# Kernel tuning notes

Hardware: AMD Instinct MI355X
Metric: run time of the kernel (lower is better)

The kernel has to match this reference:

```python
import jax, jax.numpy as jnp
import numpy as np

B, L, D, H = 4, 2048, 1024, 16
DK = D // H


def setup_inputs() -> dict:
    key = jax.random.key(0)
    ks = jax.random.split(key, 8)
    def n(k, shape, s=1.0):
        return jax.random.normal(k, shape, dtype=jnp.float32) * s
    return {
        "q": n(ks[0], (B, L, D)),
        "k": n(ks[1], (B, L, D)),
        "v": n(ks[2], (B, L, D)),
        "Wq": n(ks[3], (D, D), 0.02), "bq": jnp.zeros((D,), jnp.float32),
        "Wk": n(ks[4], (D, D), 0.02), "bk": jnp.zeros((D,), jnp.float32),
        "Wv": n(ks[5], (D, D), 0.02), "bv": jnp.zeros((D,), jnp.float32),
        "Wo": n(ks[6], (D, D), 0.02), "bo": jnp.zeros((D,), jnp.float32),
        # relative-position table, torch: nn.Parameter(zeros(2L-1, d_k)); random here
        "w_rel": n(ks[7], (2 * L - 1, DK), 0.02),
    }


def reference(q, k, v, Wq, bq, Wk, bk, Wv, bv, Wo, bo, w_rel):
    # Dropout is identity in eval mode (reference baseline).
    bs, Lq, _ = q.shape
    qh = (q @ Wq.T + bq).reshape(bs, Lq, H, DK).transpose(0, 2, 1, 3)  # (B,H,L,dk)
    kh = (k @ Wk.T + bk).reshape(bs, -1, H, DK).transpose(0, 2, 1, 3)
    vh = (v @ Wv.T + bv).reshape(bs, -1, H, DK).transpose(0, 2, 1, 3)

    # content-content scores
    scores = jnp.einsum('bhid,bhjd->bhij', qh, kh)  # (B,H,L,L)

    # relative bias. torch unfold: rel_pos[i, d, j] = w_rel[i + j, d]
    # bias[b,h,i,j] = sum_d qh[b,h,i,d] * w_rel[i+j, d]
    # Compute t = q . w_rel over the 2L-1 axis, then skew-gather (avoids LxLxdk tensor).
    t = jnp.einsum('bhid,rd->bhir', qh, w_rel)  # (B,H,L,2L-1)
    idx = jnp.arange(Lq)[:, None] + jnp.arange(Lq)[None, :]  # (L,L) values i+j
    bias = jnp.take_along_axis(t, idx[None, None], axis=-1)  # (B,H,L,L)

    attn = jax.nn.softmax((scores + bias) / jnp.sqrt(jnp.float32(DK)), axis=-1)
    out = jnp.einsum('bhij,bhjd->bhid', attn, vh)  # (B,H,L,dk)
    concat = out.transpose(0, 2, 1, 3).reshape(bs, Lq, D)
    return concat @ Wo.T + bo
```

## Files before the change

### kernel.cpp

```cpp
#include <hip/hip_runtime.h>

typedef __attribute__((ext_vector_type(8))) short bf16x8;
typedef __attribute__((ext_vector_type(4))) float f32x4;
typedef unsigned short u16;
typedef unsigned int u32;

constexpr int kB = 4, kL = 2048, kD = 1024, kH = 16, kDK = 64;
constexpr int kR = kB * kL;
constexpr long kWrelMax = 2 * kL - 2;
constexpr float kQScale = 0.125f * 1.44269504088896f;
constexpr float kM = 12.0f;

__device__ inline float fexp2(float x) { return __builtin_amdgcn_exp2f(x); }

__device__ inline u16 f2bf(float x) {
    union { float f; u32 u; } v; v.f = x;
    u32 r = v.u + 0x7FFFu + ((v.u >> 16) & 1u);
    return (u16)(r >> 16);
}
__device__ inline float bf2f(u16 h) {
    union { u32 u; float f; } v; v.u = ((u32)h) << 16;
    return v.f;
}
__device__ inline void splitf(float x, u16& hi, u16& lo) {
    hi = f2bf(x);
    lo = f2bf(x - bf2f(hi));
}
__device__ inline f32x4 MFMA(bf16x8 a, bf16x8 b, f32x4 c) {
    return __builtin_amdgcn_mfma_f32_16x16x32_bf16(a, b, c, 0, 0, 0);
}
__device__ __forceinline__ void gll16(const u16* g, u16* l) {
    __builtin_amdgcn_global_load_lds(
        (const __attribute__((address_space(1))) u32*)g,
        (__attribute__((address_space(3))) u32*)l, 16, 0, 0);
}

__global__ void split4_kernel(const float* __restrict__ in,
                              u16* __restrict__ hi, u16* __restrict__ lo, int n4) {
    int idx = blockIdx.x * blockDim.x + threadIdx.x;
    if (idx >= n4) return;
    float4 x = reinterpret_cast<const float4*>(in)[idx];
    ushort4 h, l;
    splitf(x.x, h.x, l.x); splitf(x.y, h.y, l.y);
    splitf(x.z, h.z, l.z); splitf(x.w, h.w, l.w);
    reinterpret_cast<ushort4*>(hi)[idx] = h;
    reinterpret_cast<ushort4*>(lo)[idx] = l;
}

template<int AMODE, int OMODE, int TERMS>
__global__ __launch_bounds__(256) void mfma_gemm(
    const float* __restrict__ Af32,
    const u16* __restrict__ Agh, const u16* __restrict__ Agl,
    const u16* __restrict__ Bgh, const u16* __restrict__ Bgl,
    const float* __restrict__ bias, float scale,
    float* __restrict__ Yf, u16* __restrict__ Yh, u16* __restrict__ Yl)
{
    __shared__ __align__(16) u16 Ash[128 * 32], Asl[128 * 32];
    __shared__ __align__(16) u16 Bsh[128 * 32];
    __shared__ __align__(16) u16 Bsl[TERMS == 3 ? 128 * 32 : 8];

    const int tid = threadIdx.x;
    const int row0 = blockIdx.x * 128, col0 = blockIdx.y * 128;
    const int w = tid >> 6, lane = tid & 63;
    const int s = lane & 15, g = lane >> 4;
    const int wrow = w >> 1, wcol = w & 1;
    const int srow = tid >> 1;
    const int skq  = (tid & 1) * 16;

    const f32x4 fz = {0.f, 0.f, 0.f, 0.f};
    f32x4 acc[4][4];
    #pragma unroll
    for (int m = 0; m < 4; ++m)
        #pragma unroll
        for (int n = 0; n < 4; ++n) acc[m][n] = fz;

    float4 aR[4];
    bf16x8 aRh[2], aRl[2], bRh[2], bRl[2];

    auto loadA = [&](int k0) {
        if (AMODE == 0) {
            const float* p = &Af32[(size_t)(row0 + srow) * kD + k0 + skq];
            aR[0] = *(const float4*)(p);
            aR[1] = *(const float4*)(p + 4);
            aR[2] = *(const float4*)(p + 8);
            aR[3] = *(const float4*)(p + 12);
        } else {
            const u16* ph = &Agh[(size_t)(row0 + srow) * kD + k0 + skq];
            const u16* pl = &Agl[(size_t)(row0 + srow) * kD + k0 + skq];
            aRh[0] = *(const bf16x8*)ph; aRh[1] = *(const bf16x8*)(ph + 8);
            aRl[0] = *(const bf16x8*)pl; aRl[1] = *(const bf16x8*)(pl + 8);
        }
    };
    auto loadB = [&](int k0) {
        const u16* ph = &Bgh[(size_t)(col0 + srow) * kD + k0 + skq];
        bRh[0] = *(const bf16x8*)ph; bRh[1] = *(const bf16x8*)(ph + 8);
        if (TERMS == 3) {
            const u16* pl = &Bgl[(size_t)(col0 + srow) * kD + k0 + skq];
            bRl[0] = *(const bf16x8*)pl; bRl[1] = *(const bf16x8*)(pl + 8);
        }
    };
    auto writeAB = [&]() {
        const int c0 = skq >> 3, sw = srow & 3;
        bf16x8 h0, h1, l0, l1;
        if (AMODE == 0) {
            const float* af = (const float*)aR;
            #pragma unroll
            for (int q = 0; q < 8; ++q) {
                u16 hh, ll;
                splitf(af[q], hh, ll);     h0[q] = (short)hh; l0[q] = (short)ll;
                splitf(af[8 + q], hh, ll); h1[q] = (short)hh; l1[q] = (short)ll;
            }
        } else { h0 = aRh[0]; h1 = aRh[1]; l0 = aRl[0]; l1 = aRl[1]; }
        *(bf16x8*)&Ash[srow * 32 + (((c0    ) ^ sw) << 3)] = h0;
        *(bf16x8*)&Ash[srow * 32 + (((c0 + 1) ^ sw) << 3)] = h1;
        *(bf16x8*)&Asl[srow * 32 + (((c0    ) ^ sw) << 3)] = l0;
        *(bf16x8*)&Asl[srow * 32 + (((c0 + 1) ^ sw) << 3)] = l1;
        *(bf16x8*)&Bsh[srow * 32 + (((c0    ) ^ sw) << 3)] = bRh[0];
        *(bf16x8*)&Bsh[srow * 32 + (((c0 + 1) ^ sw) << 3)] = bRh[1];
        if (TERMS == 3) {
            *(bf16x8*)&Bsl[srow * 32 + (((c0    ) ^ sw) << 3)] = bRl[0];
            *(bf16x8*)&Bsl[srow * 32 + (((c0 + 1) ^ sw) << 3)] = bRl[1];
        }
    };

    loadA(0); loadB(0);
    for (int k0 = 0; k0 < kD; k0 += 32) {
        __syncthreads();
        writeAB();
        __syncthreads();
        if (k0 + 32 < kD) { loadA(k0 + 32); loadB(k0 + 32); }

        bf16x8 fAh[4], fAl[4], fBh[4], fBl[4];
        #pragma unroll
        for (int m = 0; m < 4; ++m) {
            int ar = wrow * 64 + m * 16 + s;
            int off = ar * 32 + ((g ^ (ar & 3)) << 3);
            fAh[m] = *(const bf16x8*)&Ash[off];
            fAl[m] = *(const bf16x8*)&Asl[off];
        }
        #pragma unroll
        for (int n = 0; n < 4; ++n) {
            int bc = wcol * 64 + n * 16 + s;
            int off = bc * 32 + ((g ^ (bc & 3)) << 3);
            fBh[n] = *(const bf16x8*)&Bsh[off];
            if (TERMS == 3) fBl[n] = *(const bf16x8*)&Bsl[off];
        }
        #pragma unroll
        for (int m = 0; m < 4; ++m)
            #pragma unroll
            for (int n = 0; n < 4; ++n) {
                acc[m][n] = MFMA(fAh[m], fBh[n], acc[m][n]);
                acc[m][n] = MFMA(fAl[m], fBh[n], acc[m][n]);
                if (TERMS == 3) acc[m][n] = MFMA(fAh[m], fBl[n], acc[m][n]);
            }
    }

    #pragma unroll
    for (int n = 0; n < 4; ++n) {
        const int colg = col0 + wcol * 64 + n * 16 + s;
        const float bv = bias[colg];
        #pragma unroll
        for (int m = 0; m < 4; ++m) {
            const int rowg = row0 + wrow * 64 + m * 16 + (g << 2);
            #pragma unroll
            for (int r = 0; r < 4; ++r) {
                float val = (acc[m][n][r] + bv) * scale;
                if (OMODE == 1) {
                    Yf[(size_t)(rowg + r) * kD + colg] = val;
                } else {
                    const int rg = rowg + r;
                    const int b = rg >> 11, i = rg & (kL - 1);
                    const int h = colg >> 6, d = colg & 63;
                    size_t o = (((size_t)b * kH + h) * kL + i) * kDK + d;
                    if (OMODE == 0) { u16 hh, ll; splitf(val, hh, ll); Yh[o] = hh; Yl[o] = ll; }
                    else             { Yh[o] = f2bf(val); }
                }
            }
        }
    }
}

__global__ __launch_bounds__(256) void transpose64(const u16* __restrict__ src,
                                                   u16* __restrict__ dst) {
    __shared__ u16 tls[64][72];
    const int tid = threadIdx.x;
    const int bh = blockIdx.y, j0 = blockIdx.x * 64;
    const int jr = tid >> 2, d0 = (tid & 3) * 16;
    const u16* p = src + ((size_t)bh * kL + j0 + jr) * kDK + d0;
    *(bf16x8*)&tls[jr][d0]     = *(const bf16x8*)p;
    *(bf16x8*)&tls[jr][d0 + 8] = *(const bf16x8*)(p + 8);
    __syncthreads();
    const int dr = tid >> 2, jc = (tid & 3) * 16;
    __align__(16) u16 tmp[16];
    #pragma unroll
    for (int q = 0; q < 16; ++q) tmp[q] = tls[jc + q][dr];
    u16* pd = dst + ((size_t)bh * kDK + dr) * kL + j0 + jc;
    *(bf16x8*)pd       = *(const bf16x8*)&tmp[0];
    *(bf16x8*)(pd + 8) = *(const bf16x8*)&tmp[8];
}

__global__ __launch_bounds__(256, 2) void attn3(
    const u16* __restrict__ Qh,
    const u16* __restrict__ Kg, const u16* __restrict__ VT,
    const u16* __restrict__ Wr,
    u16* __restrict__ Ch, u16* __restrict__ Cl)
{
    __shared__ __align__(16) u16 Ksh[2][64 * 64];
    __shared__ __align__(16) u16 Vsh[2][64 * 64];
    __shared__ __align__(16) u16 Wsh[2][64 * 64];
    __shared__ __align__(16) u16 Ps[4][16 * 64];
    __shared__ __align__(16) u16 Tb[4][128 * 20];

    const int tid = threadIdx.x;
    const int w = tid >> 6, lane = tid & 63;
    const int s = lane & 15, g = lane >> 4;
    const int bh = blockIdx.y, i0 = blockIdx.x * 64;
    const int b = bh >> 4, h = bh & 15;

    const int srow = tid >> 3;
    const int sc = tid & 7;

    auto stageK = [&](int buf, int t) {
        const u16* base = Kg + ((size_t)bh * kL + (size_t)t * 64) * kDK;
        #pragma unroll
        for (int it = 0; it < 2; ++it) {
            int r = srow + it * 32;
            gll16(base + r * 64 + ((sc ^ (r & 7)) << 3), &Ksh[buf][it * 2048 + w * 512]);
        }
    };
    auto stageV = [&](int buf, int t) {
        #pragma unroll
        for (int it = 0; it < 2; ++it) {
            int d = srow + it * 32;
            const u16* src = VT + ((size_t)bh * kDK + d) * kL + t * 64 + ((sc ^ (d & 7)) << 3);
            gll16(src, &Vsh[buf][it * 2048 + w * 512]);
        }
    };
    auto stageW = [&](int buf, int c) {
        #pragma unroll
        for (int it = 0; it < 2; ++it) {
            int r = srow + it * 32;
            long row = (long)i0 + 64L * c + r;
            if (row > kWrelMax) row = kWrelMax;
            gll16(Wr + row * 64 + ((sc ^ (r & 7)) << 3), &Wsh[buf][it * 2048 + w * 512]);
        }
    };

    int foff[4][2];
    #pragma unroll
    for (int n = 0; n < 4; ++n)
        #pragma unroll
        for (int ks = 0; ks < 2; ++ks) {
            int row = n * 16 + s;
            foff[n][ks] = row * 64 + (((ks * 4 + g) ^ (row & 7)) << 3);
        }
    int prd[2];
    #pragma unroll
    for (int ks = 0; ks < 2; ++ks)
        prd[ks] = s * 64 + (((ks * 4 + g) ^ (s & 7)) << 3);
    int pwoff[4][4];
    #pragma unroll
    for (int jn = 0; jn < 4; ++jn)
        #pragma unroll
        for (int r = 0; r < 4; ++r) {
            int il = g * 4 + r, j = jn * 16 + s;
            pwoff[jn][r] = il * 64 + (((j >> 3) ^ (il & 7)) << 3) + (j & 7);
        }

    const size_t qbase = ((size_t)bh * kL + i0 + w * 16 + s) * kDK + g * 8;
    bf16x8 qh[2];
    qh[0] = *(const bf16x8*)&Qh[qbase];
    qh[1] = *(const bf16x8*)&Qh[qbase + 32];

    auto computeT = [&](int c, int buf) {
        const f32x4 fz = {0.f, 0.f, 0.f, 0.f};
        f32x4 tacc[4] = {fz, fz, fz, fz};
        #pragma unroll
        for (int un = 0; un < 4; ++un)
            #pragma unroll
            for (int ks = 0; ks < 2; ++ks) {
                bf16x8 wf = *(const bf16x8*)&Wsh[buf][foff[un][ks]];
                tacc[un] = MFMA(qh[ks], wf, tacc[un]);
            }
        const int cb = c * 64 + s - g * 4;
        #pragma unroll
        for (int un = 0; un < 4; ++un)
            #pragma unroll
            for (int r = 0; r < 4; ++r) {
                int key = (cb + un * 16 - r) & 127;
                Tb[w][key * 20 + g * 4 + r] =
                    (u16)(__float_as_uint(tacc[un][r]) >> 16);
            }
    };

    stageK(0, 0); stageV(0, 0); stageW(0, 0); stageW(1, 1);
    __syncthreads();
    computeT(0, 0); computeT(1, 1);
    __syncthreads();

    float lS[4] = {0.f, 0.f, 0.f, 0.f};
    const f32x4 fz = {0.f, 0.f, 0.f, 0.f};
    f32x4 oacc[4] = {fz, fz, fz, fz};

    for (int t = 0; t < 32; ++t) {
        const int cur = t & 1, nxt = cur ^ 1;
        if (t < 31) {
            stageK(nxt, t + 1);
            stageV(nxt, t + 1);
            stageW(cur, t + 2);
        }
        if (t >= 1) computeT(t + 1, nxt);

        f32x4 sacc[4] = {fz, fz, fz, fz};
        #pragma unroll
        for (int jn = 0; jn < 4; ++jn)
            #pragma unroll
            for (int ks = 0; ks < 2; ++ks) {
                bf16x8 kf = *(const bf16x8*)&Ksh[cur][foff[jn][ks]];
                sacc[jn] = MFMA(qh[ks], kf, sacc[jn]);
            }

        #pragma unroll
        for (int jn = 0; jn < 4; ++jn) {
            int key = (w * 16 + t * 64 + jn * 16 + s) & 127;
            ushort4 tv = *(const ushort4*)&Tb[w][key * 20 + g * 4];
            sacc[jn][0] += bf2f(tv.x);
            sacc[jn][1] += bf2f(tv.y);
            sacc[jn][2] += bf2f(tv.z);
            sacc[jn][3] += bf2f(tv.w);
        }

        #pragma unroll
        for (int jn = 0; jn < 4; ++jn)
            #pragma unroll
            for (int r = 0; r < 4; ++r) {
                float p = fexp2(sacc[jn][r] - kM);
                u32 pu = __float_as_uint(p) & 0xFFFF0000u;
                lS[r] += __uint_as_float(pu);
                Ps[w][pwoff[jn][r]] = (u16)(pu >> 16);
            }

        #pragma unroll
        for (int ks = 0; ks < 2; ++ks) {
            bf16x8 pf = *(const bf16x8*)&Ps[w][prd[ks]];
            #pragma unroll
            for (int dn = 0; dn < 4; ++dn) {
                bf16x8 vf = *(const bf16x8*)&Vsh[cur][foff[dn][ks]];
                oacc[dn] = MFMA(pf, vf, oacc[dn]);
            }
        }
        __syncthreads();
    }

    float inv[4];
    #pragma unroll
    for (int r = 0; r < 4; ++r) {
        float ps = lS[r];
        ps += __shfl_xor(ps, 1);
        ps += __shfl_xor(ps, 2);
        ps += __shfl_xor(ps, 4);
        ps += __shfl_xor(ps, 8);
        inv[r] = 1.0f / ps;
    }
    #pragma unroll
    for (int dn = 0; dn < 4; ++dn)
        #pragma unroll
        for (int r = 0; r < 4; ++r) {
            const int ig = i0 + w * 16 + g * 4 + r;
            float val = oacc[dn][r] * inv[r];
            u16 hh, ll; splitf(val, hh, ll);
            size_t o = ((size_t)(b * kL + ig)) * kD + h * kDK + dn * 16 + s;
            Ch[o] = hh; Cl[o] = ll;
        }
}

extern "C" void kernel_launch(void* const* d_in, const int* in_sizes, int n_in,
                              void* d_out, int out_size, void* d_ws, size_t ws_size,
                              hipStream_t stream) {
    const float* q    = (const float*)d_in[0];
    const float* k    = (const float*)d_in[1];
    const float* v    = (const float*)d_in[2];
    const float* Wq   = (const float*)d_in[3];
    const float* bq   = (const float*)d_in[4];
    const float* Wk   = (const float*)d_in[5];
    const float* bk   = (const float*)d_in[6];
    const float* Wv   = (const float*)d_in[7];
    const float* bv   = (const float*)d_in[8];
    const float* Wo   = (const float*)d_in[9];
    const float* bo   = (const float*)d_in[10];
    const float* wrel = (const float*)d_in[11];
    float* out = (float*)d_out;

    u16* p = (u16*)d_ws;
    const size_t nW = (size_t)kD * kD;
    const size_t nR = (size_t)(2 * kL - 1) * kDK;
    const size_t nT = (size_t)kB * kL * kD;
    u16* wqh = p; p += nW;  u16* wql = p; p += nW;
    u16* wkh = p; p += nW;  u16* wkl = p; p += nW;
    u16* wvh = p; p += nW;  u16* wvl = p; p += nW;
    u16* woh = p; p += nW;  u16* wol = p; p += nW;
    u16* wrh = p; p += nR;  u16* wrl = p; p += nR;
    u16* qhh = p; p += nT;
    u16* khh = p; p += nT;
    u16* vhh = p; p += nT;
    u16* vT  = p; p += nT;
    u16* cch = p; p += nT;  u16* ccl = p; p += nT;

    hipLaunchKernelGGL(split4_kernel, dim3(1024), dim3(256), 0, stream, Wq, wqh, wql, (int)(nW / 4));
    hipLaunchKernelGGL(split4_kernel, dim3(1024), dim3(256), 0, stream, Wk, wkh, wkl, (int)(nW / 4));
    hipLaunchKernelGGL(split4_kernel, dim3(1024), dim3(256), 0, stream, Wv, wvh, wvl, (int)(nW / 4));
    hipLaunchKernelGGL(split4_kernel, dim3(1024), dim3(256), 0, stream, Wo, woh, wol, (int)(nW / 4));
    hipLaunchKernelGGL(split4_kernel, dim3(256),  dim3(256), 0, stream, wrel, wrh, wrl, (int)(nR / 4));

    dim3 blk(256);
    dim3 gP(kR / 128, kD / 128);
    hipLaunchKernelGGL((mfma_gemm<0, 2, 2>), gP, blk, 0, stream,
                       q, nullptr, nullptr, wqh, wql, bq, kQScale, nullptr, qhh, nullptr);
    hipLaunchKernelGGL((mfma_gemm<0, 2, 2>), gP, blk, 0, stream,
                       k, nullptr, nullptr, wkh, wkl, bk, 1.0f, nullptr, khh, nullptr);
    hipLaunchKernelGGL((mfma_gemm<0, 2, 2>), gP, blk, 0, stream,
                       v, nullptr, nullptr, wvh, wvl, bv, 1.0f, nullptr, vhh, nullptr);

    hipLaunchKernelGGL(transpose64, dim3(kL / 64, kB * kH), blk, 0, stream, vhh, vT);

    hipLaunchKernelGGL(attn3, dim3(kL / 64, kB * kH), blk, 0, stream,
                       qhh, khh, vT, wrh, cch, ccl);

    hipLaunchKernelGGL((mfma_gemm<1, 1, 3>), gP, blk, 0, stream,
                       nullptr, cch, ccl, woh, wol, bo, 1.0f, out, nullptr, nullptr);
}
```

Baseline: 449.3 us.

## Fuse V transpose into projection epilogue, batch weight splits, add MFMA priority

The V projection now writes its bf16 output directly in transposed (d-major) layout, which removes the separate transpose kernel and its intermediate buffer. The four weight split launches are merged into one 2D-grid kernel, and splitf now truncates instead of rounding for the hi part. In the attention loop, s_setprio raises wave priority around the MFMA blocks. The transposed stores are 8-byte writes with a large stride, which may coalesce poorly, and truncating the hi part changes how the error is split between hi and lo.

```diff
diff --git a/kernel.cpp b/kernel.cpp
--- a/kernel.cpp
+++ b/kernel.cpp
@@ -23,8 +23,12 @@
     return v.f;
 }
 __device__ inline void splitf(float x, u16& hi, u16& lo) {
-    hi = f2bf(x);
-    lo = f2bf(x - bf2f(hi));
+    union { float f; u32 u; } v; v.f = x;
+    u32 hu = v.u & 0xFFFF0000u;
+    hi = (u16)(hu >> 16);
+    union { u32 u; float f; } hf; hf.u = hu;
+    union { float f; u32 u; } l; l.f = x - hf.f;
+    lo = (u16)(l.u >> 16);
 }
 __device__ inline f32x4 MFMA(bf16x8 a, bf16x8 b, f32x4 c) {
     return __builtin_amdgcn_mfma_f32_16x16x32_bf16(a, b, c, 0, 0, 0);
@@ -35,6 +39,24 @@
         (__attribute__((address_space(3))) u32*)l, 16, 0, 0);
 }
 
+__global__ void split4x4_kernel(const float* __restrict__ i0, const float* __restrict__ i1,
+                                const float* __restrict__ i2, const float* __restrict__ i3,
+                                u16* __restrict__ h0, u16* __restrict__ h1,
+                                u16* __restrict__ h2, u16* __restrict__ h3,
+                                u16* __restrict__ l0, u16* __restrict__ l1,
+                                u16* __restrict__ l2, u16* __restrict__ l3, int n4) {
+    int idx = blockIdx.x * blockDim.x + threadIdx.x;
+    if (idx >= n4) return;
+    const float* in = blockIdx.y == 0 ? i0 : blockIdx.y == 1 ? i1 : blockIdx.y == 2 ? i2 : i3;
+    u16* hi = blockIdx.y == 0 ? h0 : blockIdx.y == 1 ? h1 : blockIdx.y == 2 ? h2 : h3;
+    u16* lo = blockIdx.y == 0 ? l0 : blockIdx.y == 1 ? l1 : blockIdx.y == 2 ? l2 : l3;
+    float4 x = reinterpret_cast<const float4*>(in)[idx];
+    ushort4 h, l;
+    splitf(x.x, h.x, l.x); splitf(x.y, h.y, l.y);
+    splitf(x.z, h.z, l.z); splitf(x.w, h.w, l.w);
+    reinterpret_cast<ushort4*>(hi)[idx] = h;
+    reinterpret_cast<ushort4*>(lo)[idx] = l;
+}
 __global__ void split4_kernel(const float* __restrict__ in,
                               u16* __restrict__ hi, u16* __restrict__ lo, int n4) {
     int idx = blockIdx.x * blockDim.x + threadIdx.x;
@@ -162,41 +184,32 @@
         #pragma unroll
         for (int m = 0; m < 4; ++m) {
             const int rowg = row0 + wrow * 64 + m * 16 + (g << 2);
-            #pragma unroll
-            for (int r = 0; r < 4; ++r) {
-                float val = (acc[m][n][r] + bv) * scale;
-                if (OMODE == 1) {
-                    Yf[(size_t)(rowg + r) * kD + colg] = val;
-                } else {
-                    const int rg = rowg + r;
-                    const int b = rg >> 11, i = rg & (kL - 1);
-                    const int h = colg >> 6, d = colg & 63;
-                    size_t o = (((size_t)b * kH + h) * kL + i) * kDK + d;
-                    if (OMODE == 0) { u16 hh, ll; splitf(val, hh, ll); Yh[o] = hh; Yl[o] = ll; }
-                    else             { Yh[o] = f2bf(val); }
+            if (OMODE == 3) {
+                const int b = rowg >> 11, i = rowg & (kL - 1);
+                const int h = colg >> 6, d = colg & 63;
+                ushort4 o4;
+                o4.x = f2bf(acc[m][n][0] + bv);
+                o4.y = f2bf(acc[m][n][1] + bv);
+                o4.z = f2bf(acc[m][n][2] + bv);
+                o4.w = f2bf(acc[m][n][3] + bv);
+                *(ushort4*)&Yh[(((size_t)b * kH + h) * kDK + d) * kL + i] = o4;
+            } else {
+                #pragma unroll
+                for (int r = 0; r < 4; ++r) {
+                    float val = (acc[m][n][r] + bv) * scale;
+                    if (OMODE == 1) {
+                        Yf[(size_t)(rowg + r) * kD + colg] = val;
+                    } else {
+                        const int rg = rowg + r;
+                        const int b = rg >> 11, i = rg & (kL - 1);
+                        const int h = colg >> 6, d = colg & 63;
+                        size_t o = (((size_t)b * kH + h) * kL + i) * kDK + d;
+                        Yh[o] = f2bf(val);
+                    }
                 }
             }
         }
     }
-}
-
-__global__ __launch_bounds__(256) void transpose64(const u16* __restrict__ src,
-                                                   u16* __restrict__ dst) {
-    __shared__ u16 tls[64][72];
-    const int tid = threadIdx.x;
-    const int bh = blockIdx.y, j0 = blockIdx.x * 64;
-    const int jr = tid >> 2, d0 = (tid & 3) * 16;
-    const u16* p = src + ((size_t)bh * kL + j0 + jr) * kDK + d0;
-    *(bf16x8*)&tls[jr][d0]     = *(const bf16x8*)p;
-    *(bf16x8*)&tls[jr][d0 + 8] = *(const bf16x8*)(p + 8);
-    __syncthreads();
-    const int dr = tid >> 2, jc = (tid & 3) * 16;
-    __align__(16) u16 tmp[16];
-    #pragma unroll
-    for (int q = 0; q < 16; ++q) tmp[q] = tls[jc + q][dr];
-    u16* pd = dst + ((size_t)bh * kDK + dr) * kL + j0 + jc;
-    *(bf16x8*)pd       = *(const bf16x8*)&tmp[0];
-    *(bf16x8*)(pd + 8) = *(const bf16x8*)&tmp[8];
 }
 
 __global__ __launch_bounds__(256, 2) void attn3(
@@ -312,6 +325,7 @@
         if (t >= 1) computeT(t + 1, nxt);
 
         f32x4 sacc[4] = {fz, fz, fz, fz};
+        __builtin_amdgcn_s_setprio(1);
         #pragma unroll
         for (int jn = 0; jn < 4; ++jn)
             #pragma unroll
@@ -319,6 +333,7 @@
                 bf16x8 kf = *(const bf16x8*)&Ksh[cur][foff[jn][ks]];
                 sacc[jn] = MFMA(qh[ks], kf, sacc[jn]);
             }
+        __builtin_amdgcn_s_setprio(0);
 
         #pragma unroll
         for (int jn = 0; jn < 4; ++jn) {
@@ -340,6 +355,7 @@
                 Ps[w][pwoff[jn][r]] = (u16)(pu >> 16);
             }
 
+        __builtin_amdgcn_s_setprio(1);
         #pragma unroll
         for (int ks = 0; ks < 2; ++ks) {
             bf16x8 pf = *(const bf16x8*)&Ps[w][prd[ks]];
@@ -349,6 +365,7 @@
                 oacc[dn] = MFMA(pf, vf, oacc[dn]);
             }
         }
+        __builtin_amdgcn_s_setprio(0);
         __syncthreads();
     }
 
@@ -402,15 +419,14 @@
     u16* wrh = p; p += nR;  u16* wrl = p; p += nR;
     u16* qhh = p; p += nT;
     u16* khh = p; p += nT;
-    u16* vhh = p; p += nT;
     u16* vT  = p; p += nT;
     u16* cch = p; p += nT;  u16* ccl = p; p += nT;
 
-    hipLaunchKernelGGL(split4_kernel, dim3(1024), dim3(256), 0, stream, Wq, wqh, wql, (int)(nW / 4));
-    hipLaunchKernelGGL(split4_kernel, dim3(1024), dim3(256), 0, stream, Wk, wkh, wkl, (int)(nW / 4));
-    hipLaunchKernelGGL(split4_kernel, dim3(1024), dim3(256), 0, stream, Wv, wvh, wvl, (int)(nW / 4));
-    hipLaunchKernelGGL(split4_kernel, dim3(1024), dim3(256), 0, stream, Wo, woh, wol, (int)(nW / 4));
-    hipLaunchKernelGGL(split4_kernel, dim3(256),  dim3(256), 0, stream, wrel, wrh, wrl, (int)(nR / 4));
+    hipLaunchKernelGGL(split4x4_kernel, dim3(1024, 4), dim3(256), 0, stream,
+                       Wq, Wk, Wv, Wo, wqh, wkh, wvh, woh, wql, wkl, wvl, wol,
+                       (int)(nW / 4));
+    hipLaunchKernelGGL(split4_kernel, dim3(256), dim3(256), 0, stream,
+                       wrel, wrh, wrl, (int)(nR / 4));
 
     dim3 blk(256);
     dim3 gP(kR / 128, kD / 128);
@@ -418,10 +434,8 @@
                        q, nullptr, nullptr, wqh, wql, bq, kQScale, nullptr, qhh, nullptr);
     hipLaunchKernelGGL((mfma_gemm<0, 2, 2>), gP, blk, 0, stream,
                        k, nullptr, nullptr, wkh, wkl, bk, 1.0f, nullptr, khh, nullptr);
-    hipLaunchKernelGGL((mfma_gemm<0, 2, 2>), gP, blk, 0, stream,
-                       v, nullptr, nullptr, wvh, wvl, bv, 1.0f, nullptr, vhh, nullptr);
-
-    hipLaunchKernelGGL(transpose64, dim3(kL / 64, kB * kH), blk, 0, stream, vhh, vT);
+    hipLaunchKernelGGL((mfma_gemm<0, 3, 2>), gP, blk, 0, stream,
+                       v, nullptr, nullptr, wvh, wvl, bv, 1.0f, nullptr, vT, nullptr);
 
     hipLaunchKernelGGL(attn3, dim3(kL / 64, kB * kH), blk, 0, stream,
                        qhh, khh, vT, wrh, cch, ccl);
```

After: 409.8 us. 1.1x faster.
